# Optimization experiments

Measured on AMD Instinct MI355X. Metric: run time of the kernel, lower is better.

The kernel has to match this reference:

```python
import jax, jax.numpy as jnp
import numpy as np

K = 5  # hard-coded neighbor count in get_graph_feature


def _graph_feature(x):
    # x: (B, C, N) -> (B, 2C, N, K)
    xt = jnp.swapaxes(x, 1, 2)                      # (B, N, C)
    sq = jnp.sum(xt * xt, axis=-1)                  # (B, N)
    inner = jnp.einsum('bnc,bmc->bnm', xt, xt)      # (B, N, N)
    pdist = 2.0 * inner - sq[:, :, None] - sq[:, None, :]  # -||xi-xj||^2
    idx = jax.lax.top_k(pdist, K)[1]                # (B, N, K) nearest (incl self)
    nbr = jax.vmap(lambda f, i: f[i])(xt, idx)      # (B, N, K, C) gather
    ctr = jnp.broadcast_to(xt[:, :, None, :], nbr.shape)
    feat = jnp.concatenate([nbr, ctr], axis=-1)     # (B, N, K, 2C)
    return jnp.transpose(feat, (0, 3, 1, 2))        # (B, 2C, N, K)


def _conv1x1(w, x):
    # w: (Cout, Cin), x: (B, Cin, N, K)
    return jnp.einsum('oc,bcnk->bonk', w, x)


def setup_inputs() -> dict:
    key = jax.random.key(0)
    ks = jax.random.split(key, 6)
    B, N = 4, 8192
    x = jax.random.normal(ks[0], (B, 3, N), dtype=jnp.float32)

    def xavier(k, cout, cin):
        std = (2.0 / (cin + cout)) ** 0.5
        return std * jax.random.normal(k, (cout, cin), dtype=jnp.float32)

    return {
        'x': x,
        'w1': xavier(ks[1], 64, 6),
        'w2': xavier(ks[2], 64, 64),
        'w3': xavier(ks[3], 128, 64),
        'w4': xavier(ks[4], 256, 128),
        'w5': xavier(ks[5], 512, 512),
    }


def reference(x, w1, w2, w3, w4, w5):
    B, _, N = x.shape
    h = _graph_feature(x)                           # (B, 6, N, K)
    h = jax.nn.relu(_conv1x1(w1, h))
    x1 = jnp.max(h, axis=-1, keepdims=True)         # (B, 64, N, 1)
    h = jax.nn.relu(_conv1x1(w2, h))
    x2 = jnp.max(h, axis=-1, keepdims=True)         # (B, 64, N, 1)
    h = jax.nn.relu(_conv1x1(w3, h))
    x3 = jnp.max(h, axis=-1, keepdims=True)         # (B, 128, N, 1)
    h = jax.nn.relu(_conv1x1(w4, h))
    x4 = jnp.max(h, axis=-1, keepdims=True)         # (B, 256, N, 1)
    cat = jnp.concatenate([x1, x2, x3, x4], axis=1) # (B, 512, N, 1)
    out = jax.nn.relu(_conv1x1(w5, cat))            # (B, 512, N, 1)
    return out.reshape(B, -1, N)
```

## Files before the change

### kernel.cpp

```cpp
#include <hip/hip_runtime.h>
#include <cstdint>

#define BATCH 4
#define NPTS  8192
#define KNN   5
#define CAPQ  64

typedef short bf16x8 __attribute__((ext_vector_type(8)));
typedef float f32x4  __attribute__((ext_vector_type(4)));
#define MFMA16(a, b, c) __builtin_amdgcn_mfma_f32_16x16x32_bf16((a), (b), (c), 0, 0, 0)

__device__ __forceinline__ unsigned short f2bf(float x) {
    unsigned u = __float_as_uint(x);
    unsigned r = u + 0x7fffu + ((u >> 16) & 1u);
    return (unsigned short)(r >> 16);
}
__device__ __forceinline__ float bf2f(unsigned short h) {
    return __uint_as_float(((unsigned)h) << 16);
}

__global__ __launch_bounds__(256) void wsplit_kernel(
        const float* __restrict__ w3, const float* __restrict__ w4,
        const float* __restrict__ w5, const float* __restrict__ x,
        unsigned short* __restrict__ w3H, unsigned short* __restrict__ w3L,
        unsigned short* __restrict__ w4H, unsigned short* __restrict__ w4L,
        unsigned short* __restrict__ w5H, unsigned short* __restrict__ w5L,
        float* __restrict__ c2) {
    const int i = blockIdx.x * 256 + threadIdx.x;
    if (i >= 303104) {
        const int pt = i - 303104;
        const int b = pt >> 13, n = pt & 8191;
        const float* xb = x + (size_t)b * 3 * NPTS;
        const float cx = xb[n], cy = xb[NPTS + n], cz = xb[2 * NPTS + n];
        c2[pt] = fmaf(cz, cz, fmaf(cy, cy, cx * cx));
        return;
    }
    const float* src; unsigned short *dh, *dl; int off;
    if (i < 8192)       { src = w3; dh = w3H; dl = w3L; off = i; }
    else if (i < 40960) { src = w4; dh = w4H; dl = w4L; off = i - 8192; }
    else                { src = w5; dh = w5H; dl = w5L; off = i - 40960; }
    const float v = src[off];
    const unsigned short hi = f2bf(v);
    dh[off] = hi;
    dl[off] = f2bf(v - bf2f(hi));
}

__global__ __launch_bounds__(512) void knn_kernel(const float* __restrict__ x,
                                                  const float* __restrict__ c2,
                                                  int* __restrict__ idx_out) {
    __shared__ __align__(16) char sbuf[32768];
    __shared__ float  thrA[8 * 64];
    __shared__ float  thrQ[64];
    __shared__ int    qcnt[64];
    __shared__ int    qidx[64 * CAPQ];

    const int t = threadIdx.x;
    const int lane = t & 63;
    const int s = t >> 6;
    const int b = blockIdx.x >> 7;
    const int q0 = (blockIdx.x & 127) * 64;
    const int qg = q0 + lane;
    const float* xb = x + (size_t)b * 3 * NPTS;

    float4* stw = ((float4*)sbuf) + s * 256;
    double* qd  = (double*)sbuf;

    const float nqx = -2.0f * xb[qg];
    const float nqy = -2.0f * xb[NPTS + qg];
    const float nqz = -2.0f * xb[2 * NPTS + qg];

    if (t < 64) qcnt[t] = 0;

    const float4* gx = (const float4*)xb;
    const float4* gy = (const float4*)(xb + NPTS);
    const float4* gz = (const float4*)(xb + 2 * NPTS);
    const float4* gc = (const float4*)(c2 + b * NPTS);
    const int base4 = s * 256;

    float s0 = 3e38f, s1 = 3e38f, s2 = 3e38f, s3 = 3e38f, s4 = 3e38f;
    {
        float4 xv = gx[base4 + lane], yv = gy[base4 + lane];
        float4 zv = gz[base4 + lane], cv = gc[base4 + lane];
        for (int ch = 0; ch < 4; ++ch) {
            stw[0 * 64 + lane] = make_float4(xv.x, yv.x, zv.x, cv.x);
            stw[1 * 64 + lane] = make_float4(xv.y, yv.y, zv.y, cv.y);
            stw[2 * 64 + lane] = make_float4(xv.z, yv.z, zv.z, cv.z);
            stw[3 * 64 + lane] = make_float4(xv.w, yv.w, zv.w, cv.w);
            if (ch < 3) {
                const int f4 = base4 + (ch + 1) * 64 + lane;
                xv = gx[f4]; yv = gy[f4]; zv = gz[f4]; cv = gc[f4];
            }
            for (int u8 = 0; u8 < 32; ++u8) {
                float4 cd[8];
                #pragma unroll
                for (int j = 0; j < 8; ++j) cd[j] = stw[u8 * 8 + j];
                #pragma unroll
                for (int j = 0; j < 8; ++j) {
                    const float dj = fmaf(cd[j].x, nqx,
                                     fmaf(cd[j].y, nqy,
                                     fmaf(cd[j].z, nqz, cd[j].w)));
                    s4 = __builtin_amdgcn_fmed3f(s3, dj, s4);
                    s3 = __builtin_amdgcn_fmed3f(s2, dj, s3);
                    s2 = __builtin_amdgcn_fmed3f(s1, dj, s2);
                    s1 = __builtin_amdgcn_fmed3f(s0, dj, s1);
                    s0 = fminf(s0, dj);
                }
            }
        }
    }
    thrA[s * 64 + lane] = s4;
    __syncthreads();
    if (t < 64) {
        float m = thrA[t];
        #pragma unroll
        for (int ww = 1; ww < 8; ++ww) m = fminf(m, thrA[ww * 64 + t]);
        thrQ[t] = m + 4e-4f;
    }
    __syncthreads();

    const float thrq = thrQ[lane];
    {
        float4 xv = gx[base4 + lane], yv = gy[base4 + lane];
        float4 zv = gz[base4 + lane], cv = gc[base4 + lane];
        for (int ch = 0; ch < 4; ++ch) {
            const int cb = s * 1024 + ch * 256;
            stw[0 * 64 + lane] = make_float4(xv.x, yv.x, zv.x, cv.x);
            stw[1 * 64 + lane] = make_float4(xv.y, yv.y, zv.y, cv.y);
            stw[2 * 64 + lane] = make_float4(xv.z, yv.z, zv.z, cv.z);
            stw[3 * 64 + lane] = make_float4(xv.w, yv.w, zv.w, cv.w);
            if (ch < 3) {
                const int f4 = base4 + (ch + 1) * 64 + lane;
                xv = gx[f4]; yv = gy[f4]; zv = gz[f4]; cv = gc[f4];
            }
            for (int u8 = 0; u8 < 32; ++u8) {
                float4 cd[8];
                #pragma unroll
                for (int j = 0; j < 8; ++j) cd[j] = stw[u8 * 8 + j];
                #pragma unroll
                for (int j = 0; j < 8; ++j) {
                    const float dj = fmaf(cd[j].x, nqx,
                                     fmaf(cd[j].y, nqy,
                                     fmaf(cd[j].z, nqz, cd[j].w)));
                    if (dj < thrq) {
                        const int slot = atomicAdd(&qcnt[lane], 1);
                        const int u = u8 * 8 + j;
                        const int gid = cb + 4 * (u & 63) + (u >> 6);
                        if (slot < CAPQ) qidx[lane * CAPQ + slot] = gid;
                    }
                }
            }
        }
    }
    __syncthreads();

    const int ql = t >> 3;
    const int jt = t & 7;
    const int cnt = min(qcnt[ql], CAPQ);
    const double Qx = (double)xb[q0 + ql];
    const double Qy = (double)xb[NPTS + q0 + ql];
    const double Qz = (double)xb[2 * NPTS + q0 + ql];
    for (int j = jt; j < cnt; j += 8) {
        const int ci = qidx[ql * CAPQ + j];
        const double ddx = Qx - (double)xb[ci];
        const double ddy = Qy - (double)xb[NPTS + ci];
        const double ddz = Qz - (double)xb[2 * NPTS + ci];
        qd[ql * CAPQ + j] = ddx * ddx + ddy * ddy + ddz * ddz;
    }
    __syncthreads();
    for (int j = jt; j < cnt; j += 8) {
        const double dj = qd[ql * CAPQ + j];
        const int    ij = qidx[ql * CAPQ + j];
        int rank = 0;
        for (int k = 0; k < cnt; ++k) {
            const double dk = qd[ql * CAPQ + k];
            const int    ik = qidx[ql * CAPQ + k];
            rank += (dk < dj) || (dk == dj && ik < ij);
        }
        if (rank < KNN)
            idx_out[((size_t)b * NPTS + q0 + ql) * KNN + rank] = ij;
    }
}

__global__ __launch_bounds__(256) void mlp12_kernel(const float* __restrict__ x,
                                                    const int* __restrict__ idx,
                                                    const float* __restrict__ w1,
                                                    const float* __restrict__ w2,
                                                    unsigned short* __restrict__ h2HL,
                                                    unsigned short* __restrict__ catH,
                                                    unsigned short* __restrict__ catL) {
    __shared__ float w1s[64 * 6];
    __shared__ float w2s[64 * 68];
    __shared__ float fbuf[80][6];
    __shared__ float h1s[80 * 68];
    __shared__ float h2s[80 * 68];
    const int t = threadIdx.x;
    const int pbase = blockIdx.x * 16;

    for (int i = t; i < 384; i += 256) w1s[i] = w1[i];
    for (int i = t; i < 4096; i += 256) {
        int c = i >> 6, q = i & 63;
        w2s[c * 68 + q] = w2[i];
    }
    if (t < 80) {
        const int pt = pbase + t / 5;
        const int b = pt >> 13;
        const int n = pt & 8191;
        const int k = t % 5;
        const int j = idx[(size_t)pt * KNN + k];
        const float* xb = x + (size_t)b * 3 * NPTS;
        fbuf[t][0] = xb[j];
        fbuf[t][1] = xb[NPTS + j];
        fbuf[t][2] = xb[2 * NPTS + j];
        fbuf[t][3] = xb[n];
        fbuf[t][4] = xb[NPTS + n];
        fbuf[t][5] = xb[2 * NPTS + n];
    }
    __syncthreads();

    for (int o = t; o < 5120; o += 256) {
        const int r = o >> 6, c = o & 63;
        float acc = 0.f;
        #pragma unroll
        for (int q = 0; q < 6; ++q) acc = fmaf(w1s[c * 6 + q], fbuf[r][q], acc);
        h1s[r * 68 + c] = fmaxf(acc, 0.f);
    }
    __syncthreads();

    for (int o = t; o < 1024; o += 256) {
        const int p = o >> 6, c = o & 63;
        float m = h1s[(p * 5) * 68 + c];
        #pragma unroll
        for (int k = 1; k < 5; ++k) m = fmaxf(m, h1s[(p * 5 + k) * 68 + c]);
        const unsigned short hi = f2bf(m);
        const size_t co = (size_t)(pbase + p) * 512 + c;
        catH[co] = hi;
        catL[co] = f2bf(m - bf2f(hi));
    }

    for (int tile = t; tile < 320; tile += 256) {
        const int r0 = (tile % 20) * 4;
        const int c0 = (tile / 20) * 4;
        float acc[4][4] = {};
        for (int q = 0; q < 64; q += 4) {
            float4 a[4], w[4];
            #pragma unroll
            for (int i = 0; i < 4; ++i) a[i] = *(const float4*)&h1s[(r0 + i) * 68 + q];
            #pragma unroll
            for (int j = 0; j < 4; ++j) w[j] = *(const float4*)&w2s[(c0 + j) * 68 + q];
            #pragma unroll
            for (int i = 0; i < 4; ++i)
                #pragma unroll
                for (int j = 0; j < 4; ++j) {
                    acc[i][j] = fmaf(a[i].x, w[j].x, acc[i][j]);
                    acc[i][j] = fmaf(a[i].y, w[j].y, acc[i][j]);
                    acc[i][j] = fmaf(a[i].z, w[j].z, acc[i][j]);
                    acc[i][j] = fmaf(a[i].w, w[j].w, acc[i][j]);
                }
        }
        #pragma unroll
        for (int i = 0; i < 4; ++i)
            #pragma unroll
            for (int j = 0; j < 4; ++j)
                h2s[(r0 + i) * 68 + c0 + j] = fmaxf(acc[i][j], 0.f);
    }
    __syncthreads();

    for (int o = t; o < 1024; o += 256) {
        const int p = o >> 6, c = o & 63;
        float m = h2s[(p * 5) * 68 + c];
        #pragma unroll
        for (int k = 1; k < 5; ++k) m = fmaxf(m, h2s[(p * 5 + k) * 68 + c]);
        const unsigned short hi = f2bf(m);
        const size_t co = (size_t)(pbase + p) * 512 + 64 + c;
        catH[co] = hi;
        catL[co] = f2bf(m - bf2f(hi));
    }
    for (int o = t; o < 5120; o += 256) {
        const int r = o >> 6, c = o & 63;
        const float v = h2s[r * 68 + c];
        const unsigned short hi = f2bf(v);
        const size_t rowb = (size_t)(pbase * 5 + r) * 128;
        h2HL[rowb + c]      = hi;
        h2HL[rowb + 64 + c] = f2bf(v - bf2f(hi));
    }
}

__global__ __launch_bounds__(256) void mlp3_kernel(
        const unsigned short* __restrict__ h2HL,
        const unsigned short* __restrict__ w3H, const unsigned short* __restrict__ w3L,
        unsigned short* __restrict__ h3H, unsigned short* __restrict__ h3L,
        unsigned short* __restrict__ catH, unsigned short* __restrict__ catL) {
    __shared__ __align__(16) char smem[59904];
    unsigned short* aH = (unsigned short*)smem;
    unsigned short* aL = aH + 80 * 72;
    unsigned short* bH = (unsigned short*)(smem + 23040);
    unsigned short* bL = (unsigned short*)(smem + 41472);

    const int t = threadIdx.x;
    const int R0 = blockIdx.x * 80;
    const int P0 = blockIdx.x * 16;

    for (int c = t; c < 1280; c += 256) {
        const int row = c >> 4, seg = c & 15;
        const uint4 v = *(const uint4*)(h2HL + (size_t)(R0 + row) * 128 + seg * 8);
        *(uint4*)((seg < 8 ? aH : aL) + row * 72 + (seg & 7) * 8) = v;
    }
    for (int c = t; c < 1024; c += 256) {
        const int row = c >> 3, seg = c & 7;
        *(uint4*)(bH + row * 72 + seg * 8) =
            *(const uint4*)(w3H + row * 64 + seg * 8);
    }
    for (int c = t; c < 1024; c += 256) {
        const int row = c >> 3, seg = c & 7;
        *(uint4*)(bL + row * 72 + seg * 8) =
            *(const uint4*)(w3L + row * 64 + seg * 8);
    }
    __syncthreads();

    const int w = t >> 6, lane = t & 63;
    const int q = lane >> 4, l16 = lane & 15;
    const int n0 = w * 32;

    f32x4 acc[5][2];
    #pragma unroll
    for (int mt = 0; mt < 5; ++mt)
        #pragma unroll
        for (int nt = 0; nt < 2; ++nt)
            acc[mt][nt] = (f32x4){0.f, 0.f, 0.f, 0.f};

    #pragma unroll
    for (int kt = 0; kt < 2; ++kt) {
        const int k0 = kt * 32 + q * 8;
        bf16x8 bh[2], bl[2];
        #pragma unroll
        for (int nt = 0; nt < 2; ++nt) {
            bh[nt] = *(const bf16x8*)(bH + (n0 + nt * 16 + l16) * 72 + k0);
            bl[nt] = *(const bf16x8*)(bL + (n0 + nt * 16 + l16) * 72 + k0);
        }
        #pragma unroll
        for (int mt = 0; mt < 5; ++mt) {
            const bf16x8 ah = *(const bf16x8*)(aH + (mt * 16 + l16) * 72 + k0);
            const bf16x8 al = *(const bf16x8*)(aL + (mt * 16 + l16) * 72 + k0);
            #pragma unroll
            for (int nt = 0; nt < 2; ++nt) {
                acc[mt][nt] = MFMA16(ah, bh[nt], acc[mt][nt]);
                acc[mt][nt] = MFMA16(ah, bl[nt], acc[mt][nt]);
                acc[mt][nt] = MFMA16(al, bh[nt], acc[mt][nt]);
            }
        }
    }

    __syncthreads();
    float* Dbuf = (float*)smem;
    #pragma unroll
    for (int mt = 0; mt < 5; ++mt)
        #pragma unroll
        for (int nt = 0; nt < 2; ++nt)
            #pragma unroll
            for (int r = 0; r < 4; ++r)
                Dbuf[(mt * 16 + q * 4 + r) * 132 + n0 + nt * 16 + l16] =
                    fmaxf(acc[mt][nt][r], 0.f);
    __syncthreads();

    {
        const int col = t & 127;
        const int p0 = (t >> 7) * 8;
        #pragma unroll
        for (int p = 0; p < 8; ++p) {
            const int pp = p0 + p;
            float mx = 0.f;
            #pragma unroll
            for (int k = 0; k < 5; ++k) {
                const int row = pp * 5 + k;
                const float v = Dbuf[row * 132 + col];
                const unsigned short hi = f2bf(v);
                const unsigned short lo = f2bf(v - bf2f(hi));
                const size_t off = (size_t)(R0 + row) * 128 + col;
                h3H[off] = hi;
                h3L[off] = lo;
                mx = fmaxf(mx, bf2f(hi) + bf2f(lo));
            }
            const unsigned short mh = f2bf(mx);
            const size_t co = (size_t)(P0 + pp) * 512 + 128 + col;
            catH[co] = mh;
            catL[co] = f2bf(mx - bf2f(mh));
        }
    }
}

__global__ __launch_bounds__(256) void mlp4_kernel(
        const unsigned short* __restrict__ h3H, const unsigned short* __restrict__ h3L,
        const unsigned short* __restrict__ w4H, const unsigned short* __restrict__ w4L,
        unsigned short* __restrict__ catH, unsigned short* __restrict__ catL) {
    __shared__ __align__(16) char smem[64000];
    unsigned short* aH = (unsigned short*)smem;
    unsigned short* aL = aH + 80 * 136;
    unsigned short* bH = (unsigned short*)(smem + 43520);
    unsigned short* bL = (unsigned short*)(smem + 53760);

    const int t = threadIdx.x;
    const int R0 = blockIdx.x * 80;
    const int P0 = blockIdx.x * 16;
    const int ny = blockIdx.y;

    for (int c = t; c < 1280; c += 256) {
        const int row = c >> 4, seg = c & 15;
        *(uint4*)(aH + row * 136 + seg * 8) =
            *(const uint4*)(h3H + (size_t)(R0 + row) * 128 + seg * 8);
    }
    for (int c = t; c < 1280; c += 256) {
        const int row = c >> 4, seg = c & 15;
        *(uint4*)(aL + row * 136 + seg * 8) =
            *(const uint4*)(h3L + (size_t)(R0 + row) * 128 + seg * 8);
    }

    const int w = t >> 6, lane = t & 63;
    const int q = lane >> 4, l16 = lane & 15;
    const int n0 = w * 32;

    f32x4 acc[5][2];
    #pragma unroll
    for (int mt = 0; mt < 5; ++mt)
        #pragma unroll
        for (int nt = 0; nt < 2; ++nt)
            acc[mt][nt] = (f32x4){0.f, 0.f, 0.f, 0.f};

    for (int ks = 0; ks < 4; ++ks) {
        __syncthreads();
        #pragma unroll
        for (int i = 0; i < 2; ++i) {
            const int c = t + i * 256;
            const int row = c >> 2, seg = c & 3;
            *(uint4*)(bH + row * 40 + seg * 8) =
                *(const uint4*)(w4H + (size_t)(ny * 128 + row) * 128 + ks * 32 + seg * 8);
        }
        #pragma unroll
        for (int i = 0; i < 2; ++i) {
            const int c = t + i * 256;
            const int row = c >> 2, seg = c & 3;
            *(uint4*)(bL + row * 40 + seg * 8) =
                *(const uint4*)(w4L + (size_t)(ny * 128 + row) * 128 + ks * 32 + seg * 8);
        }
        __syncthreads();

        const int k0 = ks * 32 + q * 8;
        const int kb = q * 8;
        bf16x8 bh[2], bl[2];
        #pragma unroll
        for (int nt = 0; nt < 2; ++nt) {
            bh[nt] = *(const bf16x8*)(bH + (n0 + nt * 16 + l16) * 40 + kb);
            bl[nt] = *(const bf16x8*)(bL + (n0 + nt * 16 + l16) * 40 + kb);
        }
        #pragma unroll
        for (int mt = 0; mt < 5; ++mt) {
            const bf16x8 ah = *(const bf16x8*)(aH + (mt * 16 + l16) * 136 + k0);
            const bf16x8 al = *(const bf16x8*)(aL + (mt * 16 + l16) * 136 + k0);
            #pragma unroll
            for (int nt = 0; nt < 2; ++nt) {
                acc[mt][nt] = MFMA16(ah, bh[nt], acc[mt][nt]);
                acc[mt][nt] = MFMA16(ah, bl[nt], acc[mt][nt]);
                acc[mt][nt] = MFMA16(al, bh[nt], acc[mt][nt]);
            }
        }
    }

    __syncthreads();
    float* Dbuf = (float*)smem;
    #pragma unroll
    for (int mt = 0; mt < 5; ++mt)
        #pragma unroll
        for (int nt = 0; nt < 2; ++nt)
            #pragma unroll
            for (int r = 0; r < 4; ++r)
                Dbuf[(mt * 16 + q * 4 + r) * 132 + n0 + nt * 16 + l16] =
                    fmaxf(acc[mt][nt][r], 0.f);
    __syncthreads();

    {
        const int col = t & 127;
        const int p0 = (t >> 7) * 8;
        const int cout = 256 + ny * 128 + col;
        #pragma unroll
        for (int p = 0; p < 8; ++p) {
            const int pp = p0 + p;
            float mx = 0.f;
            #pragma unroll
            for (int k = 0; k < 5; ++k)
                mx = fmaxf(mx, Dbuf[(pp * 5 + k) * 132 + col]);
            const unsigned short mh = f2bf(mx);
            const size_t co = (size_t)(P0 + pp) * 512 + cout;
            catH[co] = mh;
            catL[co] = f2bf(mx - bf2f(mh));
        }
    }
}

__global__ __launch_bounds__(256) void gemm512_kernel(
        const unsigned short* __restrict__ catH, const unsigned short* __restrict__ catL,
        const unsigned short* __restrict__ w5H, const unsigned short* __restrict__ w5L,
        float* __restrict__ out) {
    __shared__ __align__(16) char smem[40960];
    unsigned short* aH = (unsigned short*)smem;
    unsigned short* aL = aH + 128 * 40;
    unsigned short* bH = (unsigned short*)(smem + 20480);
    unsigned short* bL = (unsigned short*)(smem + 30720);

    const int t = threadIdx.x;
    const int m0 = blockIdx.x * 128;
    const int n0blk = blockIdx.y * 128;

    const int w = t >> 6, lane = t & 63;
    const int q = lane >> 4, l16 = lane & 15;
    const int m_off = (w >> 1) * 64;
    const int n_off = (w & 1) * 64;

    f32x4 acc[4][4];
    #pragma unroll
    for (int mt = 0; mt < 4; ++mt)
        #pragma unroll
        for (int nt = 0; nt < 4; ++nt)
            acc[mt][nt] = (f32x4){0.f, 0.f, 0.f, 0.f};

    for (int kc = 0; kc < 512; kc += 32) {
        __syncthreads();
        #pragma unroll
        for (int i = 0; i < 2; ++i) {
            const int c = t + i * 256;
            const int row = c >> 2, seg = c & 3;
            *(uint4*)(aH + row * 40 + seg * 8) =
                *(const uint4*)(catH + (size_t)(m0 + row) * 512 + kc + seg * 8);
        }
        #pragma unroll
        for (int i = 0; i < 2; ++i) {
            const int c = t + i * 256;
            const int row = c >> 2, seg = c & 3;
            *(uint4*)(aL + row * 40 + seg * 8) =
                *(const uint4*)(catL + (size_t)(m0 + row) * 512 + kc + seg * 8);
        }
        #pragma unroll
        for (int i = 0; i < 2; ++i) {
            const int c = t + i * 256;
            const int row = c >> 2, seg = c & 3;
            *(uint4*)(bH + row * 40 + seg * 8) =
                *(const uint4*)(w5H + (size_t)(n0blk + row) * 512 + kc + seg * 8);
        }
        #pragma unroll
        for (int i = 0; i < 2; ++i) {
            const int c = t + i * 256;
            const int row = c >> 2, seg = c & 3;
            *(uint4*)(bL + row * 40 + seg * 8) =
                *(const uint4*)(w5L + (size_t)(n0blk + row) * 512 + kc + seg * 8);
        }
        __syncthreads();

        const int k0 = q * 8;
        bf16x8 bh[4], bl[4];
        #pragma unroll
        for (int nt = 0; nt < 4; ++nt) {
            bh[nt] = *(const bf16x8*)(bH + (n_off + nt * 16 + l16) * 40 + k0);
            bl[nt] = *(const bf16x8*)(bL + (n_off + nt * 16 + l16) * 40 + k0);
        }
        #pragma unroll
        for (int mt = 0; mt < 4; ++mt) {
            const bf16x8 ah = *(const bf16x8*)(aH + (m_off + mt * 16 + l16) * 40 + k0);
            const bf16x8 al = *(const bf16x8*)(aL + (m_off + mt * 16 + l16) * 40 + k0);
            #pragma unroll
            for (int nt = 0; nt < 4; ++nt) {
                acc[mt][nt] = MFMA16(ah, bh[nt], acc[mt][nt]);
                acc[mt][nt] = MFMA16(ah, bl[nt], acc[mt][nt]);
                acc[mt][nt] = MFMA16(al, bh[nt], acc[mt][nt]);
            }
        }
    }

    float* bandbuf = (float*)smem;
    for (int b8 = 0; b8 < 8; ++b8) {
        __syncthreads();
        if ((w >> 1) == (b8 >> 2)) {
            const int mt = b8 & 3;
            #pragma unroll
            for (int nt = 0; nt < 4; ++nt)
                #pragma unroll
                for (int r = 0; r < 4; ++r)
                    bandbuf[(q * 4 + r) * 132 + n_off + nt * 16 + l16] =
                        fmaxf(acc[mt][nt][r], 0.f);
        }
        __syncthreads();
        const int col = t >> 1;
        const int ph = (t & 1) * 8;
        const int P = m0 + b8 * 16 + ph;
        const int bb = P >> 13, nn = P & 8191;
        const int cout = n0blk + col;
        float tmp[8];
        #pragma unroll
        for (int j = 0; j < 8; ++j) tmp[j] = bandbuf[(ph + j) * 132 + col];
        float* op = &out[((size_t)bb * 512 + cout) * NPTS + nn];
        *(float4*)op       = make_float4(tmp[0], tmp[1], tmp[2], tmp[3]);
        *(float4*)(op + 4) = make_float4(tmp[4], tmp[5], tmp[6], tmp[7]);
    }
}

extern "C" void kernel_launch(void* const* d_in, const int* in_sizes, int n_in,
                              void* d_out, int out_size, void* d_ws, size_t ws_size,
                              hipStream_t stream) {
    (void)in_sizes; (void)n_in; (void)out_size; (void)ws_size;
    const float* x  = (const float*)d_in[0];
    const float* w1 = (const float*)d_in[1];
    const float* w2 = (const float*)d_in[2];
    const float* w3 = (const float*)d_in[3];
    const float* w4 = (const float*)d_in[4];
    const float* w5 = (const float*)d_in[5];
    float* out = (float*)d_out;

    char* ws = (char*)d_ws;
    unsigned short* w3H = (unsigned short*)(ws + 0);
    unsigned short* w3L = (unsigned short*)(ws + 16384);
    unsigned short* w4H = (unsigned short*)(ws + 32768);
    unsigned short* w4L = (unsigned short*)(ws + 98304);
    unsigned short* w5H = (unsigned short*)(ws + 163840);
    unsigned short* w5L = (unsigned short*)(ws + 688128);
    int*            idx = (int*)(ws + 1212416);
    unsigned short* catH = (unsigned short*)(ws + 2097152);
    unsigned short* catL = (unsigned short*)(ws + 35651584);
    unsigned short* h3H  = (unsigned short*)(ws + 69206016);
    float*          c2d  = (float*)(ws + 111149056);
    unsigned short* h2HL = (unsigned short*)d_out;
    unsigned short* h3L  = (unsigned short*)d_out;

    wsplit_kernel<<<dim3(1312), dim3(256), 0, stream>>>(w3, w4, w5, x,
                                                        w3H, w3L, w4H, w4L, w5H, w5L,
                                                        c2d);
    knn_kernel<<<dim3(BATCH * NPTS / 64), dim3(512), 0, stream>>>(x, c2d, idx);
    mlp12_kernel<<<dim3(BATCH * NPTS / 16), dim3(256), 0, stream>>>(x, idx, w1, w2,
                                                                    h2HL, catH, catL);
    mlp3_kernel<<<dim3(BATCH * NPTS * KNN / 80), dim3(256), 0, stream>>>(
        h2HL, w3H, w3L, h3H, h3L, catH, catL);
    mlp4_kernel<<<dim3(BATCH * NPTS * KNN / 80, 2), dim3(256), 0, stream>>>(
        h3H, h3L, w4H, w4L, catH, catL);
    gemm512_kernel<<<dim3(BATCH * NPTS / 128, 4), dim3(256), 0, stream>>>(
        catH, catL, w5H, w5L, out);
}
```

Measured before the change: 425.0 us.

## Split KNN candidate scan across 16 waves and widen refinement parallelism

After: 415.7 us. -2.2%, faster.

```diff
diff --git a/kernel.cpp b/kernel.cpp
--- a/kernel.cpp
+++ b/kernel.cpp
@@ -4,7 +4,7 @@
 #define BATCH 4
 #define NPTS  8192
 #define KNN   5
-#define CAPQ  64
+#define CAPQ  96
 
 typedef short bf16x8 __attribute__((ext_vector_type(8)));
 typedef float f32x4  __attribute__((ext_vector_type(4)));
@@ -45,11 +45,11 @@
     dl[off] = f2bf(v - bf2f(hi));
 }
 
-__global__ __launch_bounds__(512) void knn_kernel(const float* __restrict__ x,
-                                                  const float* __restrict__ c2,
-                                                  int* __restrict__ idx_out) {
+__global__ __launch_bounds__(1024, 8) void knn_kernel(const float* __restrict__ x,
+                                                      const float* __restrict__ c2,
+                                                      int* __restrict__ idx_out) {
     __shared__ __align__(16) char sbuf[32768];
-    __shared__ float  thrA[8 * 64];
+    __shared__ float  thrA[16 * 64];
     __shared__ float  thrQ[64];
     __shared__ int    qcnt[64];
     __shared__ int    qidx[64 * CAPQ];
@@ -62,7 +62,7 @@
     const int qg = q0 + lane;
     const float* xb = x + (size_t)b * 3 * NPTS;
 
-    float4* stw = ((float4*)sbuf) + s * 256;
+    float4* stw = ((float4*)sbuf) + s * 128;
     double* qd  = (double*)sbuf;
 
     const float nqx = -2.0f * xb[qg];
@@ -71,31 +71,29 @@
 
     if (t < 64) qcnt[t] = 0;
 
-    const float4* gx = (const float4*)xb;
-    const float4* gy = (const float4*)(xb + NPTS);
-    const float4* gz = (const float4*)(xb + 2 * NPTS);
-    const float4* gc = (const float4*)(c2 + b * NPTS);
-    const int base4 = s * 256;
+    const float2* gx = (const float2*)xb;
+    const float2* gy = (const float2*)(xb + NPTS);
+    const float2* gz = (const float2*)(xb + 2 * NPTS);
+    const float2* gc = (const float2*)(c2 + b * NPTS);
+    const int f2base = s * 256;
 
     float s0 = 3e38f, s1 = 3e38f, s2 = 3e38f, s3 = 3e38f, s4 = 3e38f;
     {
-        float4 xv = gx[base4 + lane], yv = gy[base4 + lane];
-        float4 zv = gz[base4 + lane], cv = gc[base4 + lane];
+        float2 xv = gx[f2base + lane], yv = gy[f2base + lane];
+        float2 zv = gz[f2base + lane], cv = gc[f2base + lane];
         for (int ch = 0; ch < 4; ++ch) {
             stw[0 * 64 + lane] = make_float4(xv.x, yv.x, zv.x, cv.x);
             stw[1 * 64 + lane] = make_float4(xv.y, yv.y, zv.y, cv.y);
-            stw[2 * 64 + lane] = make_float4(xv.z, yv.z, zv.z, cv.z);
-            stw[3 * 64 + lane] = make_float4(xv.w, yv.w, zv.w, cv.w);
             if (ch < 3) {
-                const int f4 = base4 + (ch + 1) * 64 + lane;
-                xv = gx[f4]; yv = gy[f4]; zv = gz[f4]; cv = gc[f4];
-            }
-            for (int u8 = 0; u8 < 32; ++u8) {
-                float4 cd[8];
+                const int f2 = f2base + (ch + 1) * 64 + lane;
+                xv = gx[f2]; yv = gy[f2]; zv = gz[f2]; cv = gc[f2];
+            }
+            for (int u4 = 0; u4 < 32; ++u4) {
+                float4 cd[4];
                 #pragma unroll
-                for (int j = 0; j < 8; ++j) cd[j] = stw[u8 * 8 + j];
+                for (int j = 0; j < 4; ++j) cd[j] = stw[u4 * 4 + j];
                 #pragma unroll
-                for (int j = 0; j < 8; ++j) {
+                for (int j = 0; j < 4; ++j) {
                     const float dj = fmaf(cd[j].x, nqx,
                                      fmaf(cd[j].y, nqy,
                                      fmaf(cd[j].z, nqz, cd[j].w)));
@@ -113,71 +111,72 @@
     if (t < 64) {
         float m = thrA[t];
         #pragma unroll
-        for (int ww = 1; ww < 8; ++ww) m = fminf(m, thrA[ww * 64 + t]);
+        for (int ww = 1; ww < 16; ++ww) m = fminf(m, thrA[ww * 64 + t]);
         thrQ[t] = m + 4e-4f;
     }
     __syncthreads();
 
     const float thrq = thrQ[lane];
     {
-        float4 xv = gx[base4 + lane], yv = gy[base4 + lane];
-        float4 zv = gz[base4 + lane], cv = gc[base4 + lane];
+        float2 xv = gx[f2base + lane], yv = gy[f2base + lane];
+        float2 zv = gz[f2base + lane], cv = gc[f2base + lane];
         for (int ch = 0; ch < 4; ++ch) {
-            const int cb = s * 1024 + ch * 256;
+            const int cb = s * 512 + ch * 128;
             stw[0 * 64 + lane] = make_float4(xv.x, yv.x, zv.x, cv.x);
             stw[1 * 64 + lane] = make_float4(xv.y, yv.y, zv.y, cv.y);
-            stw[2 * 64 + lane] = make_float4(xv.z, yv.z, zv.z, cv.z);
-            stw[3 * 64 + lane] = make_float4(xv.w, yv.w, zv.w, cv.w);
             if (ch < 3) {
-                const int f4 = base4 + (ch + 1) * 64 + lane;
-                xv = gx[f4]; yv = gy[f4]; zv = gz[f4]; cv = gc[f4];
-            }
-            for (int u8 = 0; u8 < 32; ++u8) {
-                float4 cd[8];
+                const int f2 = f2base + (ch + 1) * 64 + lane;
+                xv = gx[f2]; yv = gy[f2]; zv = gz[f2]; cv = gc[f2];
+            }
+            for (int u4 = 0; u4 < 32; ++u4) {
+                float4 cd[4];
                 #pragma unroll
-                for (int j = 0; j < 8; ++j) cd[j] = stw[u8 * 8 + j];
+                for (int j = 0; j < 4; ++j) cd[j] = stw[u4 * 4 + j];
                 #pragma unroll
-                for (int j = 0; j < 8; ++j) {
+                for (int j = 0; j < 4; ++j) {
                     const float dj = fmaf(cd[j].x, nqx,
                                      fmaf(cd[j].y, nqy,
                                      fmaf(cd[j].z, nqz, cd[j].w)));
                     if (dj < thrq) {
                         const int slot = atomicAdd(&qcnt[lane], 1);
-                        const int u = u8 * 8 + j;
-                        const int gid = cb + 4 * (u & 63) + (u >> 6);
+                        const int u = u4 * 4 + j;
+                        const int gid = cb + 2 * (u & 63) + (u >> 6);
                         if (slot < CAPQ) qidx[lane * CAPQ + slot] = gid;
                     }
                 }
             }
         }
     }
-    __syncthreads();
-
-    const int ql = t >> 3;
-    const int jt = t & 7;
-    const int cnt = min(qcnt[ql], CAPQ);
-    const double Qx = (double)xb[q0 + ql];
-    const double Qy = (double)xb[NPTS + q0 + ql];
-    const double Qz = (double)xb[2 * NPTS + q0 + ql];
-    for (int j = jt; j < cnt; j += 8) {
-        const int ci = qidx[ql * CAPQ + j];
-        const double ddx = Qx - (double)xb[ci];
-        const double ddy = Qy - (double)xb[NPTS + ci];
-        const double ddz = Qz - (double)xb[2 * NPTS + ci];
-        qd[ql * CAPQ + j] = ddx * ddx + ddy * ddy + ddz * ddz;
-    }
-    __syncthreads();
-    for (int j = jt; j < cnt; j += 8) {
-        const double dj = qd[ql * CAPQ + j];
-        const int    ij = qidx[ql * CAPQ + j];
-        int rank = 0;
-        for (int k = 0; k < cnt; ++k) {
-            const double dk = qd[ql * CAPQ + k];
-            const int    ik = qidx[ql * CAPQ + k];
-            rank += (dk < dj) || (dk == dj && ik < ij);
-        }
-        if (rank < KNN)
-            idx_out[((size_t)b * NPTS + q0 + ql) * KNN + rank] = ij;
+
+    const int qll = t >> 5;
+    const int jt = t & 31;
+    for (int ph = 0; ph < 2; ++ph) {
+        __syncthreads();
+        const int ql = ph * 32 + qll;
+        const int cnt = min(qcnt[ql], CAPQ);
+        const double Qx = (double)xb[q0 + ql];
+        const double Qy = (double)xb[NPTS + q0 + ql];
+        const double Qz = (double)xb[2 * NPTS + q0 + ql];
+        for (int j = jt; j < cnt; j += 32) {
+            const int ci = qidx[ql * CAPQ + j];
+            const double ddx = Qx - (double)xb[ci];
+            const double ddy = Qy - (double)xb[NPTS + ci];
+            const double ddz = Qz - (double)xb[2 * NPTS + ci];
+            qd[qll * CAPQ + j] = ddx * ddx + ddy * ddy + ddz * ddz;
+        }
+        __syncthreads();
+        for (int j = jt; j < cnt; j += 32) {
+            const double dj = qd[qll * CAPQ + j];
+            const int    ij = qidx[ql * CAPQ + j];
+            int rank = 0;
+            for (int k = 0; k < cnt; ++k) {
+                const double dk = qd[qll * CAPQ + k];
+                const int    ik = qidx[ql * CAPQ + k];
+                rank += (dk < dj) || (dk == dj && ik < ij);
+            }
+            if (rank < KNN)
+                idx_out[((size_t)b * NPTS + q0 + ql) * KNN + rank] = ij;
+        }
     }
 }
 
@@ -630,7 +629,7 @@
     wsplit_kernel<<<dim3(1312), dim3(256), 0, stream>>>(w3, w4, w5, x,
                                                         w3H, w3L, w4H, w4L, w5H, w5L,
                                                         c2d);
-    knn_kernel<<<dim3(BATCH * NPTS / 64), dim3(512), 0, stream>>>(x, c2d, idx);
+    knn_kernel<<<dim3(BATCH * NPTS / 64), dim3(1024), 0, stream>>>(x, c2d, idx);
     mlp12_kernel<<<dim3(BATCH * NPTS / 16), dim3(256), 0, stream>>>(x, idx, w1, w2,
                                                                     h2HL, catH, catL);
     mlp3_kernel<<<dim3(BATCH * NPTS * KNN / 80), dim3(256), 0, stream>>>(
```
